# Optimization experiments

Measured on AMD Instinct MI355X. Metric: run time of the kernel, lower is better.

Reference implementation:

```python
import jax, jax.numpy as jnp
import numpy as np
from jax import lax

EPS = 1e-8
DN = ('NCHW', 'OIHW', 'NCHW')


def setup_inputs() -> dict:
    key = jax.random.key(0)
    k1, k2 = jax.random.split(key)
    inputs = jax.random.normal(k1, (16, 3, 512, 512), dtype=jnp.float32)
    template = jax.random.normal(k2, (16, 3, 21, 21), dtype=jnp.float32)
    return {"inputs": inputs, "template": template}


def _normalize_template(template):
    # Z-normalize each (batch, channel) plane independently, then divide by
    # patch element count (matches NCC.__init__).
    B, C, th, tw = template.shape
    t = template.reshape(B, C, th * tw)
    t = t - jnp.mean(t, axis=-1, keepdims=True)
    t = t / (jnp.std(t, axis=-1, keepdims=True) + EPS)  # ddof=0 == unbiased=False
    return t.reshape(B, C, th, tw) / (th * tw)


def reference(inputs, template):
    B, C, H, W = inputs.shape
    th, tw = template.shape[2], template.shape[3]
    nt = _normalize_template(template)

    # Per-(b,c) depthwise cross-correlation (the grouped conv with eye-masked
    # weights is exactly a depthwise conv with per-sample filters).
    x = inputs.reshape(1, B * C, H, W)
    w = nt.reshape(B * C, 1, th, tw)
    res = lax.conv_general_dilated(x, w, (1, 1), 'VALID',
                                   dimension_numbers=DN,
                                   feature_group_count=B * C)
    res = res.reshape(B, C, res.shape[2], res.shape[3])  # (B,C,Hout,Wout)

    # Local (patch) std per channel via box filter (shared across batch).
    box = jnp.full((C, 1, th, tw), 1.0 / (th * tw), dtype=inputs.dtype)
    mean = lax.conv_general_dilated(inputs, box, (1, 1), 'VALID',
                                    dimension_numbers=DN, feature_group_count=C)
    mean_sq = lax.conv_general_dilated(inputs * inputs, box, (1, 1), 'VALID',
                                       dimension_numbers=DN, feature_group_count=C)
    std = jnp.sqrt(mean_sq - mean * mean + EPS)

    return res / (std + EPS)
```

## Files before the change

### kernel.cpp

```cpp
#include <hip/hip_runtime.h>
#include <math.h>

typedef __attribute__((ext_vector_type(8)))  short short8;
typedef __attribute__((ext_vector_type(16))) float f32x16;

#define NPLANE 48
#define H 512
#define W 512
#define TH 21
#define OH 492
#define OW 492
#define EPSF 1e-8f

#define BONES_HOFF (4128768u / 2)
#define V_HOFF     (4194304u / 2)
#define V2_HOFF    (29360128u / 2)

__device__ inline unsigned short f2bf(float f) {
    unsigned u = __float_as_uint(f);
    return (unsigned short)((u + 0x7FFFu + ((u >> 16) & 1u)) >> 16);
}

__global__ void build_b_kernel(const float* __restrict__ tpl,
                               unsigned short* __restrict__ ws16) {
    __shared__ float sm[2];
    const int plane = blockIdx.x;
    const float* t = tpl + plane * 441;
    const int tid = threadIdx.x;
    if (tid < 64) {
        float s = 0.f, s2 = 0.f;
        for (int k = tid; k < 441; k += 64) {
            float x = t[k];
            s += x; s2 += x * x;
        }
#pragma unroll
        for (int o = 32; o >= 1; o >>= 1) {
            s  += __shfl_down(s, o);
            s2 += __shfl_down(s2, o);
        }
        if (tid == 0) {
            float mean = s / 441.f;
            float var = fmaxf(s2 / 441.f - mean * mean, 0.f);
            sm[0] = mean;
            sm[1] = 1.f / ((sqrtf(var) + EPSF) * 441.f);
        }
    }
    __syncthreads();
    const float mean = sm[0], scale = sm[1];

    unsigned short* bc = ws16 + (size_t)plane * 43008;
    for (int i = tid; i < 43008; i += 256) {
        int j = i & 7, lane = (i >> 3) & 63, s = (i >> 9) & 3, u = i >> 11;
        int k = ((lane >> 5) << 3) + j, n = lane & 31;
        int v = 16 * s + k - n;
        float val = (v >= 0 && v < TH) ? (t[u * 21 + v] - mean) * scale : 0.f;
        bc[i] = f2bf(val);
    }
    if (plane == 0) {
        unsigned short* bo = ws16 + BONES_HOFF;
        const unsigned short one = f2bf(1.f);
        for (int i = tid; i < 2048; i += 256) {
            int j = i & 7, lane = (i >> 3) & 63, s = (i >> 9) & 3;
            int k = ((lane >> 5) << 3) + j, n = lane & 31;
            int v = 16 * s + k - n;
            bo[i] = (v >= 0 && v < TH) ? one : (unsigned short)0;
        }
    }
}

#define VBAND 31
__global__ __launch_bounds__(256) void vert_kernel(
    const float* __restrict__ in, unsigned short* __restrict__ ws16) {
    const int band = blockIdx.x;
    const int cg = blockIdx.y;
    const int plane = blockIdx.z;
    const int x = cg * 256 + threadIdx.x;
    const float* src = in + (size_t)plane * H * W;
    unsigned short* V  = ws16 + V_HOFF  + (size_t)plane * H * W;
    unsigned short* V2 = ws16 + V2_HOFF + (size_t)plane * H * W;

    const int y0 = band * VBAND;
    const int ylim = min(y0 + VBAND, OH);

    float s = 0.f, q = 0.f;
#pragma unroll
    for (int r = 0; r < 20; ++r) {
        float v = src[(y0 + r) * W + x];
        s += v;
        q = fmaf(v, v, q);
    }
    for (int y = y0; y < ylim; ++y) {
        float v = src[(y + 20) * W + x];
        s += v;
        q = fmaf(v, v, q);
        V[y * W + x] = f2bf(s);
        V2[y * W + x] = f2bf(q);
        float o = src[y * W + x];
        s -= o;
        q = fmaf(-o, o, q);
    }
}

__global__ __launch_bounds__(256, 3) void ncc_mfma_kernel(
    const float* __restrict__ in, const unsigned short* __restrict__ ws16,
    float* __restrict__ out) {
    __shared__ short seg[148 * 168];

    const int plane = blockIdx.z;
    const int x0 = blockIdx.x * 128;
    const int y0 = blockIdx.y * 128;
    const int tid = threadIdx.x;
    const int lane = tid & 63;
    const int wrow = tid >> 6;
    const float* src = in + (size_t)plane * H * W;

    for (int i = tid; i < 148 * 20; i += 256) {
        int row = i / 20, s8 = i - row * 20;
        int gy = y0 + row, gx = x0 + s8 * 8;
        short8 val;
        if (gy < H && gx + 7 < W) {
            float4 a = *(const float4*)(src + gy * W + gx);
            float4 b = *(const float4*)(src + gy * W + gx + 4);
            val[0] = (short)f2bf(a.x); val[1] = (short)f2bf(a.y);
            val[2] = (short)f2bf(a.z); val[3] = (short)f2bf(a.w);
            val[4] = (short)f2bf(b.x); val[5] = (short)f2bf(b.y);
            val[6] = (short)f2bf(b.z); val[7] = (short)f2bf(b.w);
        } else {
#pragma unroll
            for (int e = 0; e < 8; ++e) {
                float xv = (gy < H && gx + e < W) ? src[gy * W + gx + e] : 0.f;
                val[e] = (short)f2bf(xv);
            }
        }
        *(short8*)&seg[row * 168 + s8 * 8] = val;
    }
    __syncthreads();

    const int m = lane & 31;
    const int half = lane >> 5;
    const int abase = (wrow * 32 + m) * 168 + half * 8;
    const unsigned short* bc = ws16 + (size_t)plane * 43008 + lane * 8;

    f32x16 acc[4];
#pragma unroll
    for (int T = 0; T < 4; ++T)
#pragma unroll
        for (int e = 0; e < 16; ++e) acc[T][e] = 0.f;

    short8 bf[4], bfn[4];
#pragma unroll
    for (int s = 0; s < 4; ++s)
        bf[s] = *(const short8*)(bc + s * 512);

    for (int u = 0; u < TH; ++u) {
        const int un = (u + 1 < TH) ? u + 1 : 0;
#pragma unroll
        for (int s = 0; s < 4; ++s)
            bfn[s] = *(const short8*)(bc + (un * 4 + s) * 512);

        short8 af[10];
#pragma unroll
        for (int g = 0; g < 10; ++g)
            af[g] = *(const short8*)&seg[abase + u * 168 + g * 16];

#pragma unroll
        for (int T = 0; T < 4; ++T) {
#pragma unroll
            for (int s = 0; s < 4; ++s)
                acc[T] = __builtin_amdgcn_mfma_f32_32x32x16_bf16(
                    af[2 * T + s], bf[s], acc[T], 0, 0, 0);
        }
#pragma unroll
        for (int s = 0; s < 4; ++s) bf[s] = bfn[s];
    }

    const unsigned short* bo16 = ws16 + BONES_HOFF + lane * 8;
    short8 bones[4];
#pragma unroll
    for (int s = 0; s < 4; ++s)
        bones[s] = *(const short8*)(bo16 + s * 512);

    const unsigned short* Vp  = ws16 + V_HOFF  + (size_t)plane * H * W;
    const unsigned short* V2p = ws16 + V2_HOFF + (size_t)plane * H * W;
    const int py = min(y0 + wrow * 32 + m, OH - 1);
    const float invn = 1.f / 441.f;
    float* outp = out + (size_t)plane * OH * OW;

#pragma unroll
    for (int T = 0; T < 4; ++T) {
        const int cx = x0 + T * 32;
        f32x16 aS, aQ;
#pragma unroll
        for (int e = 0; e < 16; ++e) { aS[e] = 0.f; aQ[e] = 0.f; }
#pragma unroll
        for (int s = 0; s < 4; ++s) {
            short8 vf = *(const short8*)(Vp  + py * W + cx + s * 16 + half * 8);
            aS = __builtin_amdgcn_mfma_f32_32x32x16_bf16(vf, bones[s], aS, 0, 0, 0);
            short8 qf = *(const short8*)(V2p + py * W + cx + s * 16 + half * 8);
            aQ = __builtin_amdgcn_mfma_f32_32x32x16_bf16(qf, bones[s], aQ, 0, 0, 0);
        }
        const int gx = cx + (lane & 31);
        if (gx < OW) {
#pragma unroll
            for (int r = 0; r < 16; ++r) {
                int gy = y0 + wrow * 32 + (r & 3) + ((r >> 2) << 3) + ((lane >> 5) << 2);
                if (gy < OH) {
                    float mean = aS[r] * invn;
                    float msq  = aQ[r] * invn;
                    float sd = sqrtf(msq - mean * mean + EPSF);
                    outp[(size_t)gy * OW + gx] = acc[T][r] / (sd + EPSF);
                }
            }
        }
    }
}

extern "C" void kernel_launch(void* const* d_in, const int* in_sizes, int n_in,
                              void* d_out, int out_size, void* d_ws,
                              size_t ws_size, hipStream_t stream) {
    const float* inputs = (const float*)d_in[0];
    const float* tmpl = (const float*)d_in[1];
    float* out = (float*)d_out;
    unsigned short* ws16 = (unsigned short*)d_ws;

    build_b_kernel<<<NPLANE, 256, 0, stream>>>(tmpl, ws16);
    vert_kernel<<<dim3(16, 2, NPLANE), 256, 0, stream>>>(inputs, ws16);
    ncc_mfma_kernel<<<dim3(4, 4, NPLANE), 256, 0, stream>>>(inputs, ws16, out);
}
```

Before: 191.4 us.

## Fuse vertical box sums into NCC kernel using shared-memory tiles

```diff
diff --git a/kernel.cpp b/kernel.cpp
--- a/kernel.cpp
+++ b/kernel.cpp
@@ -12,13 +12,17 @@
 #define OW 492
 #define EPSF 1e-8f
 
+#define STRIDE 168
+#define SEG_ROWS 84
+
 #define BONES_HOFF (4128768u / 2)
-#define V_HOFF     (4194304u / 2)
-#define V2_HOFF    (29360128u / 2)
 
 __device__ inline unsigned short f2bf(float f) {
     unsigned u = __float_as_uint(f);
     return (unsigned short)((u + 0x7FFFu + ((u >> 16) & 1u)) >> 16);
+}
+__device__ inline float bf2f(unsigned s) {
+    return __uint_as_float(s << 16);
 }
 
 __global__ void build_b_kernel(const float* __restrict__ tpl,
@@ -68,53 +72,22 @@
     }
 }
 
-#define VBAND 31
-__global__ __launch_bounds__(256) void vert_kernel(
-    const float* __restrict__ in, unsigned short* __restrict__ ws16) {
-    const int band = blockIdx.x;
-    const int cg = blockIdx.y;
-    const int plane = blockIdx.z;
-    const int x = cg * 256 + threadIdx.x;
-    const float* src = in + (size_t)plane * H * W;
-    unsigned short* V  = ws16 + V_HOFF  + (size_t)plane * H * W;
-    unsigned short* V2 = ws16 + V2_HOFF + (size_t)plane * H * W;
-
-    const int y0 = band * VBAND;
-    const int ylim = min(y0 + VBAND, OH);
-
-    float s = 0.f, q = 0.f;
-#pragma unroll
-    for (int r = 0; r < 20; ++r) {
-        float v = src[(y0 + r) * W + x];
-        s += v;
-        q = fmaf(v, v, q);
-    }
-    for (int y = y0; y < ylim; ++y) {
-        float v = src[(y + 20) * W + x];
-        s += v;
-        q = fmaf(v, v, q);
-        V[y * W + x] = f2bf(s);
-        V2[y * W + x] = f2bf(q);
-        float o = src[y * W + x];
-        s -= o;
-        q = fmaf(-o, o, q);
-    }
-}
-
-__global__ __launch_bounds__(256, 3) void ncc_mfma_kernel(
+__global__ __launch_bounds__(256, 3) void ncc_fused_kernel(
     const float* __restrict__ in, const unsigned short* __restrict__ ws16,
     float* __restrict__ out) {
-    __shared__ short seg[148 * 168];
+    __shared__ short seg[SEG_ROWS * STRIDE];
+    __shared__ short vbuf[64 * STRIDE];
 
     const int plane = blockIdx.z;
     const int x0 = blockIdx.x * 128;
-    const int y0 = blockIdx.y * 128;
+    const int y0 = blockIdx.y * 64;
     const int tid = threadIdx.x;
     const int lane = tid & 63;
-    const int wrow = tid >> 6;
+    const int tr = (tid >> 6) & 1;
+    const int tc = tid >> 7;
     const float* src = in + (size_t)plane * H * W;
 
-    for (int i = tid; i < 148 * 20; i += 256) {
+    for (int i = tid; i < SEG_ROWS * 20; i += 256) {
         int row = i / 20, s8 = i - row * 20;
         int gy = y0 + row, gx = x0 + s8 * 8;
         short8 val;
@@ -132,20 +105,20 @@
                 val[e] = (short)f2bf(xv);
             }
         }
-        *(short8*)&seg[row * 168 + s8 * 8] = val;
+        *(short8*)&seg[row * STRIDE + s8 * 8] = val;
     }
     __syncthreads();
 
     const int m = lane & 31;
     const int half = lane >> 5;
-    const int abase = (wrow * 32 + m) * 168 + half * 8;
+    const int abase = (tr * 32 + m) * STRIDE + tc * 64 + half * 8;
     const unsigned short* bc = ws16 + (size_t)plane * 43008 + lane * 8;
 
-    f32x16 acc[4];
-#pragma unroll
-    for (int T = 0; T < 4; ++T)
-#pragma unroll
-        for (int e = 0; e < 16; ++e) acc[T][e] = 0.f;
+    f32x16 acc[2];
+#pragma unroll
+    for (int t = 0; t < 2; ++t)
+#pragma unroll
+        for (int e = 0; e < 16; ++e) acc[t][e] = 0.f;
 
     short8 bf[4], bfn[4];
 #pragma unroll
@@ -158,17 +131,17 @@
         for (int s = 0; s < 4; ++s)
             bfn[s] = *(const short8*)(bc + (un * 4 + s) * 512);
 
-        short8 af[10];
-#pragma unroll
-        for (int g = 0; g < 10; ++g)
-            af[g] = *(const short8*)&seg[abase + u * 168 + g * 16];
-
-#pragma unroll
-        for (int T = 0; T < 4; ++T) {
+        short8 af[6];
+#pragma unroll
+        for (int g = 0; g < 6; ++g)
+            af[g] = *(const short8*)&seg[abase + u * STRIDE + g * 16];
+
+#pragma unroll
+        for (int t = 0; t < 2; ++t) {
 #pragma unroll
             for (int s = 0; s < 4; ++s)
-                acc[T] = __builtin_amdgcn_mfma_f32_32x32x16_bf16(
-                    af[2 * T + s], bf[s], acc[T], 0, 0, 0);
+                acc[t] = __builtin_amdgcn_mfma_f32_32x32x16_bf16(
+                    af[2 * t + s], bf[s], acc[t], 0, 0, 0);
         }
 #pragma unroll
         for (int s = 0; s < 4; ++s) bf[s] = bfn[s];
@@ -180,35 +153,92 @@
     for (int s = 0; s < 4; ++s)
         bones[s] = *(const short8*)(bo16 + s * 512);
 
-    const unsigned short* Vp  = ws16 + V_HOFF  + (size_t)plane * H * W;
-    const unsigned short* V2p = ws16 + V2_HOFF + (size_t)plane * H * W;
-    const int py = min(y0 + wrow * 32 + m, OH - 1);
+    if (tid < 160) {
+        const int hr = (tid >= 80) ? 32 : 0;
+        const int c2 = (tid % 80) * 2;
+        float s0 = 0.f, s1 = 0.f;
+#pragma unroll
+        for (int r = 0; r < 20; ++r) {
+            unsigned p = *(const unsigned*)&seg[(hr + r) * STRIDE + c2];
+            s0 += bf2f(p & 0xffffu);
+            s1 += bf2f(p >> 16);
+        }
+        for (int y = hr; y < hr + 32; ++y) {
+            unsigned p = *(const unsigned*)&seg[(y + 20) * STRIDE + c2];
+            s0 += bf2f(p & 0xffffu);
+            s1 += bf2f(p >> 16);
+            *(unsigned*)&vbuf[y * STRIDE + c2] =
+                (unsigned)f2bf(s0) | ((unsigned)f2bf(s1) << 16);
+            unsigned q = *(const unsigned*)&seg[y * STRIDE + c2];
+            s0 -= bf2f(q & 0xffffu);
+            s1 -= bf2f(q >> 16);
+        }
+    }
+    __syncthreads();
+
+    f32x16 aS[2];
+#pragma unroll
+    for (int t = 0; t < 2; ++t) {
+#pragma unroll
+        for (int e = 0; e < 16; ++e) aS[t][e] = 0.f;
+#pragma unroll
+        for (int s = 0; s < 4; ++s) {
+            short8 vf = *(const short8*)&vbuf[abase + (2 * t + s) * 16];
+            aS[t] = __builtin_amdgcn_mfma_f32_32x32x16_bf16(vf, bones[s],
+                                                            aS[t], 0, 0, 0);
+        }
+    }
+    __syncthreads();
+
+    if (tid < 160) {
+        const int hr = (tid >= 80) ? 32 : 0;
+        const int c2 = (tid % 80) * 2;
+        float s0 = 0.f, s1 = 0.f;
+#pragma unroll
+        for (int r = 0; r < 20; ++r) {
+            unsigned p = *(const unsigned*)&seg[(hr + r) * STRIDE + c2];
+            float a = bf2f(p & 0xffffu), b = bf2f(p >> 16);
+            s0 = fmaf(a, a, s0);
+            s1 = fmaf(b, b, s1);
+        }
+        for (int y = hr; y < hr + 32; ++y) {
+            unsigned p = *(const unsigned*)&seg[(y + 20) * STRIDE + c2];
+            float a = bf2f(p & 0xffffu), b = bf2f(p >> 16);
+            s0 = fmaf(a, a, s0);
+            s1 = fmaf(b, b, s1);
+            *(unsigned*)&vbuf[y * STRIDE + c2] =
+                (unsigned)f2bf(s0) | ((unsigned)f2bf(s1) << 16);
+            unsigned q = *(const unsigned*)&seg[y * STRIDE + c2];
+            float c = bf2f(q & 0xffffu), d = bf2f(q >> 16);
+            s0 = fmaf(-c, c, s0);
+            s1 = fmaf(-d, d, s1);
+        }
+    }
+    __syncthreads();
+
     const float invn = 1.f / 441.f;
     float* outp = out + (size_t)plane * OH * OW;
-
-#pragma unroll
-    for (int T = 0; T < 4; ++T) {
-        const int cx = x0 + T * 32;
-        f32x16 aS, aQ;
-#pragma unroll
-        for (int e = 0; e < 16; ++e) { aS[e] = 0.f; aQ[e] = 0.f; }
+#pragma unroll
+    for (int t = 0; t < 2; ++t) {
+        f32x16 aQ;
+#pragma unroll
+        for (int e = 0; e < 16; ++e) aQ[e] = 0.f;
 #pragma unroll
         for (int s = 0; s < 4; ++s) {
-            short8 vf = *(const short8*)(Vp  + py * W + cx + s * 16 + half * 8);
-            aS = __builtin_amdgcn_mfma_f32_32x32x16_bf16(vf, bones[s], aS, 0, 0, 0);
-            short8 qf = *(const short8*)(V2p + py * W + cx + s * 16 + half * 8);
-            aQ = __builtin_amdgcn_mfma_f32_32x32x16_bf16(qf, bones[s], aQ, 0, 0, 0);
-        }
-        const int gx = cx + (lane & 31);
+            short8 qf = *(const short8*)&vbuf[abase + (2 * t + s) * 16];
+            aQ = __builtin_amdgcn_mfma_f32_32x32x16_bf16(qf, bones[s], aQ,
+                                                         0, 0, 0);
+        }
+        const int gx = x0 + tc * 64 + t * 32 + (lane & 31);
         if (gx < OW) {
 #pragma unroll
             for (int r = 0; r < 16; ++r) {
-                int gy = y0 + wrow * 32 + (r & 3) + ((r >> 2) << 3) + ((lane >> 5) << 2);
+                int gy = y0 + tr * 32 + (r & 3) + ((r >> 2) << 3) + half * 4;
                 if (gy < OH) {
-                    float mean = aS[r] * invn;
-                    float msq  = aQ[r] * invn;
+                    float mean = aS[t][r] * invn;
+                    float msq = aQ[r] * invn;
                     float sd = sqrtf(msq - mean * mean + EPSF);
-                    outp[(size_t)gy * OW + gx] = acc[T][r] / (sd + EPSF);
+                    outp[(size_t)gy * OW + gx] = acc[t][r] / (sd + EPSF);
                 }
             }
         }
@@ -224,6 +254,5 @@
     unsigned short* ws16 = (unsigned short*)d_ws;
 
     build_b_kernel<<<NPLANE, 256, 0, stream>>>(tmpl, ws16);
-    vert_kernel<<<dim3(16, 2, NPLANE), 256, 0, stream>>>(inputs, ws16);
-    ncc_mfma_kernel<<<dim3(4, 4, NPLANE), 256, 0, stream>>>(inputs, ws16, out);
-}
+    ncc_fused_kernel<<<dim3(4, 8, NPLANE), 256, 0, stream>>>(inputs, ws16, out);
+}
```

Result: faster. 164.1 us (-14.3%).
